# Optimization experiments

Hardware: AMD Instinct MI355X
Metric: run time of the kernel (lower is better)

## Reference

```python
import jax, jax.numpy as jnp
import numpy as np

NUM_GRAPHS = 64

def _seg_max(vals, ids, num_segments):
    # segment max with empty segments mapped to 0 (PyG scatter-max convention)
    m = jax.ops.segment_max(vals, ids, num_segments=num_segments)
    return jnp.where(jnp.isfinite(m), m, 0.0)

def setup_inputs() -> dict:
    key = jax.random.key(0)
    ks = jax.random.split(key, 10)
    N, E, F, L, LIN, OUT = 50000, 800000, 128, 3, 256, 10
    x = jax.random.normal(ks[0], (N, F), dtype=jnp.float32)
    edge_index = jax.random.randint(ks[1], (2, E), 0, N, dtype=jnp.int64)
    batch = jnp.sort(jax.random.randint(ks[2], (N,), 0, NUM_GRAPHS, dtype=jnp.int64))
    s = 0.05
    Ws_self = jax.random.normal(ks[3], (L, F, F), dtype=jnp.float32) * s
    Ws_nei = jax.random.normal(ks[4], (L, F, F), dtype=jnp.float32) * s
    bs = jnp.zeros((L, F), dtype=jnp.float32)
    lin_W = jax.random.normal(ks[5], (F, LIN), dtype=jnp.float32) * s
    lin_b = jnp.zeros((LIN,), dtype=jnp.float32)
    out_W = jax.random.normal(ks[6], (LIN, OUT), dtype=jnp.float32) * s
    out_b = jnp.zeros((OUT,), dtype=jnp.float32)
    return {"x": x, "edge_index": edge_index, "batch": batch,
            "Ws_self": Ws_self, "Ws_nei": Ws_nei, "bs": bs,
            "lin_W": lin_W, "lin_b": lin_b, "out_W": out_W, "out_b": out_b}

def reference(x, edge_index, batch, Ws_self, Ws_nei, bs, lin_W, lin_b, out_W, out_b):
    N = x.shape[0]
    src, dst = edge_index[0], edge_index[1]
    L = Ws_self.shape[0]
    for l in range(L):  # small fixed layer count
        agg = _seg_max(x[src], dst, N)                 # [N, F] max-aggregated neighbor feats
        x = jax.nn.relu(agg @ Ws_nei[l] + x @ Ws_self[l] + bs[l])
    pooled = _seg_max(x, batch, NUM_GRAPHS)            # [G, F] global max pool
    h = pooled @ lin_W + lin_b                         # [G, LIN]
    return h @ out_W + out_b                           # [G, OUT]
```

## Files before the change

kernel.cpp:

```cpp
#include <hip/hip_runtime.h>
#include <float.h>

typedef __bf16 bf16x8 __attribute__((ext_vector_type(8)));
typedef float f32x4 __attribute__((ext_vector_type(4)));
typedef unsigned short ushort8 __attribute__((ext_vector_type(8)));
typedef _Float16 h8 __attribute__((ext_vector_type(8)));
typedef _Float16 h4 __attribute__((ext_vector_type(4)));

__device__ inline unsigned short f2bh(float f) {
    unsigned int u = __float_as_uint(f);
    return (unsigned short)((u + 0x7FFFu + ((u >> 16) & 1u)) >> 16);
}
__device__ inline float bh2f(unsigned short h) {
    return __uint_as_float((unsigned int)h << 16);
}
__device__ inline h4 h4max(h4 a, h4 b) {
    h4 r;
    r[0] = a[0] > b[0] ? a[0] : b[0];
    r[1] = a[1] > b[1] ? a[1] : b[1];
    r[2] = a[2] > b[2] ? a[2] : b[2];
    r[3] = a[3] > b[3] ? a[3] : b[3];
    return r;
}


__global__ void cvt16_kernel(const float* __restrict__ xin, _Float16* __restrict__ x16,
                             int total8) {
    int i = blockIdx.x * blockDim.x + threadIdx.x;
    if (i >= total8) return;
    const float4* p = reinterpret_cast<const float4*>(xin + (size_t)i * 8);
    float4 a = p[0], b = p[1];
    h8 o;
    o[0] = (_Float16)a.x; o[1] = (_Float16)a.y; o[2] = (_Float16)a.z; o[3] = (_Float16)a.w;
    o[4] = (_Float16)b.x; o[5] = (_Float16)b.y; o[6] = (_Float16)b.z; o[7] = (_Float16)b.w;
    *reinterpret_cast<h8*>(x16 + (size_t)i * 8) = o;
}


__global__ void hist_kernel(const int* __restrict__ dst, int E, int* __restrict__ cnt) {
    int e = blockIdx.x * blockDim.x + threadIdx.x;
    if (e < E) atomicAdd(&cnt[dst[e]], 1);
}

__global__ __launch_bounds__(256) void bsum_kernel(const int* __restrict__ cnt, int N,
                                                   int* __restrict__ bsum) {
    __shared__ int red[256];
    int t = threadIdx.x;
    int i = blockIdx.x * 256 + t;
    red[t] = (i < N) ? cnt[i] : 0;
    __syncthreads();
    for (int off = 128; off > 0; off >>= 1) {
        if (t < off) red[t] += red[t + off];
        __syncthreads();
    }
    if (t == 0) bsum[blockIdx.x] = red[0];
}

__global__ __launch_bounds__(256) void scan_apply_kernel(const int* __restrict__ cnt, int N,
                                                         const int* __restrict__ bsum, int nb,
                                                         int* __restrict__ row_start,
                                                         int* __restrict__ bcur) {
    __shared__ int sb[256];
    __shared__ int s[256];
    int t = threadIdx.x;
    sb[t] = (t < nb) ? bsum[t] : 0;
    int i = blockIdx.x * 256 + t;
    int v = (i < N) ? cnt[i] : 0;
    s[t] = v;
    __syncthreads();
    for (int off = 1; off < 256; off <<= 1) {
        int u0 = (t >= off) ? sb[t - off] : 0;
        int u1 = (t >= off) ? s[t - off] : 0;
        __syncthreads();
        sb[t] += u0;
        s[t] += u1;
        __syncthreads();
    }
    int base = (blockIdx.x == 0) ? 0 : sb[blockIdx.x - 1];
    int excl = base + s[t] - v;
    if (i < N) {
        row_start[i] = excl;
        if ((i & 63) == 0) bcur[i >> 6] = excl;
    }
}

#define EPB 8192

__global__ __launch_bounds__(256) void partA_kernel(const int* __restrict__ src,
                                                    const int* __restrict__ dst, int E,
                                                    int nbkt, int* __restrict__ bcur,
                                                    unsigned int* __restrict__ pk) {
    __shared__ int lh[1024];
    __shared__ int lbase[1024];
    int t = threadIdx.x;
    int e0 = blockIdx.x * EPB;
    int e1 = e0 + EPB; if (e1 > E) e1 = E;
    for (int b = t; b < nbkt; b += 256) lh[b] = 0;
    __syncthreads();
    for (int e = e0 + t; e < e1; e += 256)
        atomicAdd(&lh[dst[e] >> 6], 1);
    __syncthreads();
    for (int b = t; b < nbkt; b += 256) {
        int c = lh[b];
        lbase[b] = (c > 0) ? atomicAdd(&bcur[b], c) : 0;
        lh[b] = 0;
    }
    __syncthreads();
    for (int e = e0 + t; e < e1; e += 256) {
        int d = dst[e];
        int b = d >> 6;
        int r = atomicAdd(&lh[b], 1);
        pk[lbase[b] + r] = ((unsigned int)src[e] << 6) | (unsigned int)(d & 63);
    }
}

__global__ __launch_bounds__(256) void partB_kernel(const unsigned int* __restrict__ pk,
                                                    const int* __restrict__ row_start,
                                                    int N, int E, int* __restrict__ col) {
    __shared__ int lrs[64];
    __shared__ int lcur[64];
    int b = blockIdx.x;
    int base = b * 64;
    int t = threadIdx.x;
    if (t < 64) {
        int node = base + t;
        lrs[t] = (node < N) ? row_start[node] : E;
        lcur[t] = 0;
    }
    __syncthreads();
    int lo = row_start[base];
    int nxt = base + 64;
    int hi = (nxt < N) ? row_start[nxt] : E;
    for (int i = lo + t; i < hi; i += 256) {
        unsigned int w = pk[i];
        int dl = w & 63u;
        int s = (int)(w >> 6);
        int r = atomicAdd(&lcur[dl], 1);
        col[lrs[dl] + r] = s;
    }
}


__global__ void agg_kernel(const _Float16* __restrict__ x16,
                           const int* __restrict__ row_start, const int* __restrict__ cnt,
                           const int* __restrict__ col,
                           _Float16* __restrict__ agg16, int N) {
    int node = (blockIdx.x * blockDim.x + threadIdx.x) >> 5;
    int lane = threadIdx.x & 31;
    if (node >= N) return;
    int beg = row_start[node];
    int deg = cnt[node];
    const _Float16 NEG = (_Float16)(-65504.0f);
    h4 a0, a1, a2, a3;
    a0[0]=NEG; a0[1]=NEG; a0[2]=NEG; a0[3]=NEG;
    a1 = a0; a2 = a0; a3 = a0;
    int j = 0;
    for (; j + 4 <= deg; j += 4) {
        int s0 = col[beg + j];
        int s1 = col[beg + j + 1];
        int s2 = col[beg + j + 2];
        int s3 = col[beg + j + 3];
        h4 v0 = *reinterpret_cast<const h4*>(&x16[(size_t)s0 * 128 + lane * 4]);
        h4 v1 = *reinterpret_cast<const h4*>(&x16[(size_t)s1 * 128 + lane * 4]);
        h4 v2 = *reinterpret_cast<const h4*>(&x16[(size_t)s2 * 128 + lane * 4]);
        h4 v3 = *reinterpret_cast<const h4*>(&x16[(size_t)s3 * 128 + lane * 4]);
        a0 = h4max(a0, v0);
        a1 = h4max(a1, v1);
        a2 = h4max(a2, v2);
        a3 = h4max(a3, v3);
    }
    for (; j < deg; ++j) {
        int s0 = col[beg + j];
        h4 v0 = *reinterpret_cast<const h4*>(&x16[(size_t)s0 * 128 + lane * 4]);
        a0 = h4max(a0, v0);
    }
    a0 = h4max(h4max(a0, a1), h4max(a2, a3));
    if (deg == 0) { a0[0] = (_Float16)0.f; a0[1] = (_Float16)0.f; a0[2] = (_Float16)0.f; a0[3] = (_Float16)0.f; }
    *reinterpret_cast<h4*>(&agg16[(size_t)node * 128 + lane * 4]) = a0;
}


__global__ void wprep_kernel(const float* __restrict__ Wn, const float* __restrict__ Wsf,
                             int total, unsigned short* __restrict__ Wfh,
                             unsigned short* __restrict__ Wfl) {
    int idx = blockIdx.x * blockDim.x + threadIdx.x;
    if (idx >= total) return;
    int c = idx & 127;
    int k = (idx >> 7) & 127;
    int p = (idx >> 14) & 1;
    int l = idx >> 15;
    const float* W = p ? Wsf : Wn;
    float v = W[(size_t)l * 16384 + k * 128 + c];
    unsigned short hi = f2bh(v);
    unsigned short lo = f2bh(v - bh2f(hi));
    size_t d = ((((size_t)l * 2 + p) * 16 + (k >> 3)) * 128 + c) * 8 + (k & 7);
    Wfh[d] = hi;
    Wfl[d] = lo;
}


__global__ __launch_bounds__(256) void layer_mfma(
    const _Float16* __restrict__ agg16, const _Float16* __restrict__ xin16,
    const unsigned short* __restrict__ Wfh, const unsigned short* __restrict__ Wfl,
    const float* __restrict__ bias, _Float16* __restrict__ xout16, int N)
{
    const int lane = threadIdx.x & 63;
    const int wid  = threadIdx.x >> 6;
    const int l15  = lane & 15;
    const int lg   = lane >> 4;
    const int ch   = wid & 1;
    const int rg   = wid >> 1;
    const int row0 = blockIdx.x * 32 + rg * 16;

    f32x4 acc[4];
    #pragma unroll
    for (int nt = 0; nt < 4; ++nt) { f32x4 z = {0.f,0.f,0.f,0.f}; acc[nt] = z; }

    int rc = row0 + l15; if (rc > N - 1) rc = N - 1;

    #pragma unroll
    for (int p = 0; p < 2; ++p) {
        const _Float16* A = p ? xin16 : agg16;
        const _Float16* a = A + (size_t)rc * 128 + lg * 8;
        const unsigned short* wh0 = Wfh + p * 16384 + (size_t)(ch * 64 + l15) * 8 + lg * 1024;
        const unsigned short* wl0 = Wfl + p * 16384 + (size_t)(ch * 64 + l15) * 8 + lg * 1024;
        #pragma unroll
        for (int ks = 0; ks < 4; ++ks) {
            h8 av = *reinterpret_cast<const h8*>(a + ks * 32);
            ushort8 hh, ll;
            #pragma unroll
            for (int j = 0; j < 8; ++j) {
                float f = (float)av[j];
                unsigned short hi = f2bh(f);
                float r = f - bh2f(hi);
                hh[j] = hi;
                ll[j] = (unsigned short)(__float_as_uint(r) >> 16);
            }
            bf16x8 ah = __builtin_bit_cast(bf16x8, hh);
            bf16x8 al = __builtin_bit_cast(bf16x8, ll);
            const unsigned short* whk = wh0 + ks * 4096;
            const unsigned short* wlk = wl0 + ks * 4096;
            #pragma unroll
            for (int nt = 0; nt < 4; ++nt) {
                bf16x8 bh = *reinterpret_cast<const bf16x8*>(whk + nt * 128);
                bf16x8 bl = *reinterpret_cast<const bf16x8*>(wlk + nt * 128);
                acc[nt] = __builtin_amdgcn_mfma_f32_16x16x32_bf16(ah, bh, acc[nt], 0, 0, 0);
                acc[nt] = __builtin_amdgcn_mfma_f32_16x16x32_bf16(al, bh, acc[nt], 0, 0, 0);
                acc[nt] = __builtin_amdgcn_mfma_f32_16x16x32_bf16(ah, bl, acc[nt], 0, 0, 0);
            }
        }
    }

    #pragma unroll
    for (int nt = 0; nt < 4; ++nt) {
        int colb = ch * 64 + nt * 16 + l15;
        float bv = bias[colb];
        #pragma unroll
        for (int rr = 0; rr < 4; ++rr) {
            int row = row0 + lg * 4 + rr;
            if (row < N) {
                float o = fmaxf(acc[nt][rr] + bv, 0.f);
                xout16[(size_t)row * 128 + colb] = (_Float16)o;
            }
        }
    }
}


#define POOL_CHUNK 128

__global__ __launch_bounds__(128) void pool_kernel(const _Float16* __restrict__ x16,
                                                   const int* __restrict__ batch,
                                                   int N,
                                                   unsigned int* __restrict__ pooled) {
    int f = threadIdx.x;
    int n0 = blockIdx.x * POOL_CHUNK;
    if (n0 >= N) return;
    int n1 = n0 + POOL_CHUNK; if (n1 > N) n1 = N;
    int g = batch[n0];
    float m = 0.f;
    for (int n = n0; n < n1; ++n) {
        int bg = batch[n];
        if (bg != g) {
            atomicMax(&pooled[g * 128 + f], __float_as_uint(m));
            m = 0.f; g = bg;
        }
        m = fmaxf(m, (float)x16[(size_t)n * 128 + f]);
    }
    atomicMax(&pooled[g * 128 + f], __float_as_uint(m));
}


__global__ __launch_bounds__(256) void head_kernel(
    const float* __restrict__ pooled,
    const float* __restrict__ linW, const float* __restrict__ linb,
    const float* __restrict__ outW, const float* __restrict__ outb,
    float* __restrict__ out)
{
    __shared__ float pl[128];
    __shared__ float hrow[256];
    int g = blockIdx.x, t = threadIdx.x;
    if (t < 128) pl[t] = pooled[g * 128 + t];
    __syncthreads();
    float acc = linb[t];
    for (int k = 0; k < 128; ++k) acc += pl[k] * linW[k * 256 + t];
    hrow[t] = acc;
    __syncthreads();
    if (t < 10) {
        float o = outb[t];
        for (int k = 0; k < 256; ++k) o += hrow[k] * outW[k * 10 + t];
        out[g * 10 + t] = o;
    }
}


static inline size_t align_up(size_t v, size_t a) { return (v + a - 1) & ~(a - 1); }

extern "C" void kernel_launch(void* const* d_in, const int* in_sizes, int n_in,
                              void* d_out, int out_size, void* d_ws, size_t ws_size,
                              hipStream_t stream) {
    const float* x      = (const float*)d_in[0];
    const int*   ei     = (const int*)d_in[1];
    const int*   batch  = (const int*)d_in[2];
    const float* WsSelf = (const float*)d_in[3];
    const float* WsNei  = (const float*)d_in[4];
    const float* bsAll  = (const float*)d_in[5];
    const float* linW   = (const float*)d_in[6];
    const float* linb   = (const float*)d_in[7];
    const float* outW   = (const float*)d_in[8];
    const float* outb   = (const float*)d_in[9];

    const int N = in_sizes[0] / 128;
    const int E = in_sizes[1] / 2;
    const int L = in_sizes[3] / (128 * 128);
    const int* src = ei;
    const int* dst = ei + E;
    const int nb2 = (N + 63) / 64;

    char* w = (char*)d_ws;
    int* cnt       = (int*)w;  w += align_up((size_t)N * 4, 256);
    int* row_start = (int*)w;  w += align_up((size_t)N * 4, 256);
    int* bcur      = (int*)w;  w += align_up((size_t)nb2 * 4, 256);
    int* bsum      = (int*)w;  w += align_up(256 * 4, 256);
    unsigned int* pk = (unsigned int*)w; w += align_up((size_t)E * 4, 256);
    int* col       = (int*)w;  w += align_up((size_t)E * 4, 256);
    _Float16* agg16 = (_Float16*)w; w += align_up((size_t)N * 128 * 2, 256);
    _Float16* x16in = (_Float16*)w; w += align_up((size_t)N * 128 * 2, 256);
    _Float16* xa16  = (_Float16*)w; w += align_up((size_t)N * 128 * 2, 256);
    _Float16* xb16  = (_Float16*)w; w += align_up((size_t)N * 128 * 2, 256);
    float* pooled  = (float*)w; w += align_up((size_t)64 * 128 * 4, 256);
    unsigned short* Wfh = (unsigned short*)w; w += align_up((size_t)L * 2 * 16384 * 2, 256);
    unsigned short* Wfl = (unsigned short*)w; w += align_up((size_t)L * 2 * 16384 * 2, 256);
    (void)ws_size;

    hipMemsetAsync(cnt, 0, (size_t)N * 4, stream);
    hipMemsetAsync(pooled, 0, (size_t)64 * 128 * 4, stream);

    cvt16_kernel<<<(N * 16 + 255) / 256, 256, 0, stream>>>(x, x16in, N * 16);

    const int wtotal = L * 2 * 128 * 128;
    wprep_kernel<<<(wtotal + 255) / 256, 256, 0, stream>>>(WsNei, WsSelf, wtotal, Wfh, Wfl);

    const int nb = (N + 255) / 256;
    hist_kernel<<<(E + 255) / 256, 256, 0, stream>>>(dst, E, cnt);
    bsum_kernel<<<nb, 256, 0, stream>>>(cnt, N, bsum);
    scan_apply_kernel<<<nb, 256, 0, stream>>>(cnt, N, bsum, nb, row_start, bcur);
    partA_kernel<<<(E + EPB - 1) / EPB, 256, 0, stream>>>(src, dst, E, nb2, bcur, pk);
    partB_kernel<<<nb2, 256, 0, stream>>>(pk, row_start, N, E, col);

    const _Float16* xin16 = x16in;
    _Float16* bufs[2] = { xa16, xb16 };
    for (int l = 0; l < L; ++l) {
        agg_kernel<<<(N * 32 + 255) / 256, 256, 0, stream>>>(xin16, row_start, cnt, col, agg16, N);
        layer_mfma<<<(N + 31) / 32, 256, 0, stream>>>(
            agg16, xin16,
            Wfh + (size_t)l * 2 * 16384, Wfl + (size_t)l * 2 * 16384,
            bsAll + (size_t)l * 128, bufs[l & 1], N);
        xin16 = bufs[l & 1];
    }

    pool_kernel<<<(N + POOL_CHUNK - 1) / POOL_CHUNK, 128, 0, stream>>>(
        xin16, batch, N, (unsigned int*)pooled);
    head_kernel<<<64, 256, 0, stream>>>(pooled, linW, linb, outW, outb, (float*)d_out);
}
```

Measured before the change: 311.0 us.

## Fuse neighbor max-aggregation into MFMA layer kernel via LDS staging

Replaces the separate aggregation kernel and GEMM kernel with a single per-layer kernel. It computes the max-aggregated neighbor rows for a 32-node tile directly into shared memory, using 16 lanes per node with 8-wide fp16 loads, and stages the self rows there too before the MFMA. This removes the agg16 global round trip and one launch per layer. The two memsets are folded into existing kernels, and row_start gains a sentinel entry so degree is computed from row_start. The cost is less parallelism for the gather phase, since each block now handles 32 nodes with 256 threads, and lower occupancy from the extra LDS.

New measurement: 309.8 us. No clear change (-0.4%).

```diff
diff --git a/kernel.cpp b/kernel.cpp
--- a/kernel.cpp
+++ b/kernel.cpp
@@ -5,7 +5,6 @@
 typedef float f32x4 __attribute__((ext_vector_type(4)));
 typedef unsigned short ushort8 __attribute__((ext_vector_type(8)));
 typedef _Float16 h8 __attribute__((ext_vector_type(8)));
-typedef _Float16 h4 __attribute__((ext_vector_type(4)));
 
 __device__ inline unsigned short f2bh(float f) {
     unsigned int u = __float_as_uint(f);
@@ -14,19 +13,24 @@
 __device__ inline float bh2f(unsigned short h) {
     return __uint_as_float((unsigned int)h << 16);
 }
-__device__ inline h4 h4max(h4 a, h4 b) {
-    h4 r;
-    r[0] = a[0] > b[0] ? a[0] : b[0];
-    r[1] = a[1] > b[1] ? a[1] : b[1];
-    r[2] = a[2] > b[2] ? a[2] : b[2];
-    r[3] = a[3] > b[3] ? a[3] : b[3];
+__device__ inline h8 h8max(h8 a, h8 b) {
+    h8 r;
+    #pragma unroll
+    for (int i = 0; i < 8; ++i) r[i] = a[i] > b[i] ? a[i] : b[i];
     return r;
 }
+__device__ inline h8 h8fill(_Float16 v) {
+    h8 r;
+    #pragma unroll
+    for (int i = 0; i < 8; ++i) r[i] = v;
+    return r;
+}
 
 
 __global__ void cvt16_kernel(const float* __restrict__ xin, _Float16* __restrict__ x16,
-                             int total8) {
+                             int total8, int* __restrict__ cnt, int N) {
     int i = blockIdx.x * blockDim.x + threadIdx.x;
+    if (i < N) cnt[i] = 0;
     if (i >= total8) return;
     const float4* p = reinterpret_cast<const float4*>(xin + (size_t)i * 8);
     float4 a = p[0], b = p[1];
@@ -59,10 +63,13 @@
 __global__ __launch_bounds__(256) void scan_apply_kernel(const int* __restrict__ cnt, int N,
                                                          const int* __restrict__ bsum, int nb,
                                                          int* __restrict__ row_start,
-                                                         int* __restrict__ bcur) {
+                                                         int* __restrict__ bcur,
+                                                         unsigned int* __restrict__ pooled) {
     __shared__ int sb[256];
     __shared__ int s[256];
     int t = threadIdx.x;
+    if (blockIdx.x == 0)
+        for (int k = t; k < 64 * 128; k += 256) pooled[k] = 0u;
     sb[t] = (t < nb) ? bsum[t] : 0;
     int i = blockIdx.x * 256 + t;
     int v = (i < N) ? cnt[i] : 0;
@@ -81,6 +88,7 @@
     if (i < N) {
         row_start[i] = excl;
         if ((i & 63) == 0) bcur[i >> 6] = excl;
+        if (i == N - 1) row_start[N] = excl + v;
     }
 }
 
@@ -129,8 +137,8 @@
     }
     __syncthreads();
     int lo = row_start[base];
-    int nxt = base + 64;
-    int hi = (nxt < N) ? row_start[nxt] : E;
+    int nxt = base + 64; if (nxt > N) nxt = N;
+    int hi = row_start[nxt];
     for (int i = lo + t; i < hi; i += 256) {
         unsigned int w = pk[i];
         int dl = w & 63u;
@@ -138,45 +146,6 @@
         int r = atomicAdd(&lcur[dl], 1);
         col[lrs[dl] + r] = s;
     }
-}
-
-
-__global__ void agg_kernel(const _Float16* __restrict__ x16,
-                           const int* __restrict__ row_start, const int* __restrict__ cnt,
-                           const int* __restrict__ col,
-                           _Float16* __restrict__ agg16, int N) {
-    int node = (blockIdx.x * blockDim.x + threadIdx.x) >> 5;
-    int lane = threadIdx.x & 31;
-    if (node >= N) return;
-    int beg = row_start[node];
-    int deg = cnt[node];
-    const _Float16 NEG = (_Float16)(-65504.0f);
-    h4 a0, a1, a2, a3;
-    a0[0]=NEG; a0[1]=NEG; a0[2]=NEG; a0[3]=NEG;
-    a1 = a0; a2 = a0; a3 = a0;
-    int j = 0;
-    for (; j + 4 <= deg; j += 4) {
-        int s0 = col[beg + j];
-        int s1 = col[beg + j + 1];
-        int s2 = col[beg + j + 2];
-        int s3 = col[beg + j + 3];
-        h4 v0 = *reinterpret_cast<const h4*>(&x16[(size_t)s0 * 128 + lane * 4]);
-        h4 v1 = *reinterpret_cast<const h4*>(&x16[(size_t)s1 * 128 + lane * 4]);
-        h4 v2 = *reinterpret_cast<const h4*>(&x16[(size_t)s2 * 128 + lane * 4]);
-        h4 v3 = *reinterpret_cast<const h4*>(&x16[(size_t)s3 * 128 + lane * 4]);
-        a0 = h4max(a0, v0);
-        a1 = h4max(a1, v1);
-        a2 = h4max(a2, v2);
-        a3 = h4max(a3, v3);
-    }
-    for (; j < deg; ++j) {
-        int s0 = col[beg + j];
-        h4 v0 = *reinterpret_cast<const h4*>(&x16[(size_t)s0 * 128 + lane * 4]);
-        a0 = h4max(a0, v0);
-    }
-    a0 = h4max(h4max(a0, a1), h4max(a2, a3));
-    if (deg == 0) { a0[0] = (_Float16)0.f; a0[1] = (_Float16)0.f; a0[2] = (_Float16)0.f; a0[3] = (_Float16)0.f; }
-    *reinterpret_cast<h4*>(&agg16[(size_t)node * 128 + lane * 4]) = a0;
 }
 
 
@@ -199,34 +168,82 @@
 }
 
 
-__global__ __launch_bounds__(256) void layer_mfma(
-    const _Float16* __restrict__ agg16, const _Float16* __restrict__ xin16,
+__global__ __launch_bounds__(256) void fused_layer(
+    const _Float16* __restrict__ xin16,
+    const int* __restrict__ row_start, const int* __restrict__ col,
     const unsigned short* __restrict__ Wfh, const unsigned short* __restrict__ Wfl,
     const float* __restrict__ bias, _Float16* __restrict__ xout16, int N)
 {
-    const int lane = threadIdx.x & 63;
-    const int wid  = threadIdx.x >> 6;
+    __shared__ _Float16 lds[2 * 32 * 136];
+    const int tid = threadIdx.x;
+    const int row0 = blockIdx.x * 32;
+
+    {
+        const int g = tid >> 4;
+        const int l16 = tid & 15;
+        const _Float16* xb = xin16 + (size_t)l16 * 8;
+        #pragma unroll
+        for (int pass = 0; pass < 2; ++pass) {
+            int nl = pass * 16 + g;
+            int node = row0 + nl;
+            const _Float16 NEG = (_Float16)(-65504.0f);
+            h8 a0 = h8fill(NEG), a1 = a0, a2 = a0, a3 = a0;
+            int deg = 0;
+            if (node < N) {
+                int beg = row_start[node];
+                deg = row_start[node + 1] - beg;
+                int j = 0;
+                for (; j + 4 <= deg; j += 4) {
+                    int s0 = col[beg + j];
+                    int s1 = col[beg + j + 1];
+                    int s2 = col[beg + j + 2];
+                    int s3 = col[beg + j + 3];
+                    a0 = h8max(a0, *reinterpret_cast<const h8*>(xb + (size_t)s0 * 128));
+                    a1 = h8max(a1, *reinterpret_cast<const h8*>(xb + (size_t)s1 * 128));
+                    a2 = h8max(a2, *reinterpret_cast<const h8*>(xb + (size_t)s2 * 128));
+                    a3 = h8max(a3, *reinterpret_cast<const h8*>(xb + (size_t)s3 * 128));
+                }
+                for (; j < deg; ++j) {
+                    int s0 = col[beg + j];
+                    a0 = h8max(a0, *reinterpret_cast<const h8*>(xb + (size_t)s0 * 128));
+                }
+            }
+            a0 = h8max(h8max(a0, a1), h8max(a2, a3));
+            if (deg == 0) a0 = h8fill((_Float16)0.f);
+            *reinterpret_cast<h8*>(&lds[nl * 136 + l16 * 8]) = a0;
+        }
+    }
+    #pragma unroll
+    for (int it = 0; it < 2; ++it) {
+        int idx = tid + it * 256;
+        int r = idx >> 4;
+        int c = idx & 15;
+        int grow = row0 + r;
+        h8 v = h8fill((_Float16)0.f);
+        if (grow < N) v = *reinterpret_cast<const h8*>(&xin16[(size_t)grow * 128 + c * 8]);
+        *reinterpret_cast<h8*>(&lds[4352 + r * 136 + c * 8]) = v;
+    }
+    __syncthreads();
+
+    const int lane = tid & 63;
+    const int wid  = tid >> 6;
     const int l15  = lane & 15;
     const int lg   = lane >> 4;
     const int ch   = wid & 1;
     const int rg   = wid >> 1;
-    const int row0 = blockIdx.x * 32 + rg * 16;
 
     f32x4 acc[4];
     #pragma unroll
-    for (int nt = 0; nt < 4; ++nt) { f32x4 z = {0.f,0.f,0.f,0.f}; acc[nt] = z; }
-
-    int rc = row0 + l15; if (rc > N - 1) rc = N - 1;
+    for (int nt = 0; nt < 4; ++nt) { f32x4 z = {0.f, 0.f, 0.f, 0.f}; acc[nt] = z; }
 
     #pragma unroll
     for (int p = 0; p < 2; ++p) {
-        const _Float16* A = p ? xin16 : agg16;
-        const _Float16* a = A + (size_t)rc * 128 + lg * 8;
+        const _Float16* arow = lds + p * 4352 + (rg * 16 + l15) * 136 + lg * 8;
         const unsigned short* wh0 = Wfh + p * 16384 + (size_t)(ch * 64 + l15) * 8 + lg * 1024;
         const unsigned short* wl0 = Wfl + p * 16384 + (size_t)(ch * 64 + l15) * 8 + lg * 1024;
         #pragma unroll
         for (int ks = 0; ks < 4; ++ks) {
-            h8 av = *reinterpret_cast<const h8*>(a + ks * 32);
+            h8 av = *reinterpret_cast<const h8*>(arow + ks * 32);
             ushort8 hh, ll;
             #pragma unroll
             for (int j = 0; j < 8; ++j) {
@@ -257,7 +274,7 @@
         float bv = bias[colb];
         #pragma unroll
         for (int rr = 0; rr < 4; ++rr) {
-            int row = row0 + lg * 4 + rr;
+            int row = row0 + rg * 16 + lg * 4 + rr;
             if (row < N) {
                 float o = fmaxf(acc[nt][rr] + bv, 0.f);
                 xout16[(size_t)row * 128 + colb] = (_Float16)o;
@@ -339,12 +356,11 @@
 
     char* w = (char*)d_ws;
     int* cnt       = (int*)w;  w += align_up((size_t)N * 4, 256);
-    int* row_start = (int*)w;  w += align_up((size_t)N * 4, 256);
+    int* row_start = (int*)w;  w += align_up((size_t)(N + 1) * 4, 256);
     int* bcur      = (int*)w;  w += align_up((size_t)nb2 * 4, 256);
     int* bsum      = (int*)w;  w += align_up(256 * 4, 256);
     unsigned int* pk = (unsigned int*)w; w += align_up((size_t)E * 4, 256);
     int* col       = (int*)w;  w += align_up((size_t)E * 4, 256);
-    _Float16* agg16 = (_Float16*)w; w += align_up((size_t)N * 128 * 2, 256);
     _Float16* x16in = (_Float16*)w; w += align_up((size_t)N * 128 * 2, 256);
     _Float16* xa16  = (_Float16*)w; w += align_up((size_t)N * 128 * 2, 256);
     _Float16* xb16  = (_Float16*)w; w += align_up((size_t)N * 128 * 2, 256);
@@ -353,10 +369,7 @@
     unsigned short* Wfl = (unsigned short*)w; w += align_up((size_t)L * 2 * 16384 * 2, 256);
     (void)ws_size;
 
-    hipMemsetAsync(cnt, 0, (size_t)N * 4, stream);
-    hipMemsetAsync(pooled, 0, (size_t)64 * 128 * 4, stream);
-
-    cvt16_kernel<<<(N * 16 + 255) / 256, 256, 0, stream>>>(x, x16in, N * 16);
+    cvt16_kernel<<<(N * 16 + 255) / 256, 256, 0, stream>>>(x, x16in, N * 16, cnt, N);
 
     const int wtotal = L * 2 * 128 * 128;
     wprep_kernel<<<(wtotal + 255) / 256, 256, 0, stream>>>(WsNei, WsSelf, wtotal, Wfh, Wfl);
@@ -364,16 +377,16 @@
     const int nb = (N + 255) / 256;
     hist_kernel<<<(E + 255) / 256, 256, 0, stream>>>(dst, E, cnt);
     bsum_kernel<<<nb, 256, 0, stream>>>(cnt, N, bsum);
-    scan_apply_kernel<<<nb, 256, 0, stream>>>(cnt, N, bsum, nb, row_start, bcur);
+    scan_apply_kernel<<<nb, 256, 0, stream>>>(cnt, N, bsum, nb, row_start, bcur,
+                                              (unsigned int*)pooled);
     partA_kernel<<<(E + EPB - 1) / EPB, 256, 0, stream>>>(src, dst, E, nb2, bcur, pk);
     partB_kernel<<<nb2, 256, 0, stream>>>(pk, row_start, N, E, col);
 
     const _Float16* xin16 = x16in;
     _Float16* bufs[2] = { xa16, xb16 };
     for (int l = 0; l < L; ++l) {
-        agg_kernel<<<(N * 32 + 255) / 256, 256, 0, stream>>>(xin16, row_start, cnt, col, agg16, N);
-        layer_mfma<<<(N + 31) / 32, 256, 0, stream>>>(
-            agg16, xin16,
+        fused_layer<<<(N + 31) / 32, 256, 0, stream>>>(
+            xin16, row_start, col,
             Wfh + (size_t)l * 2 * 16384, Wfl + (size_t)l * 2 * 16384,
             bsAll + (size_t)l * 128, bufs[l & 1], N);
         xin16 = bufs[l & 1];
```
